# Kernel optimization log

Hardware: AMD Instinct MI355X
Metric: run time of the kernel (lower is better)

Reference implementation:

```python
import jax, jax.numpy as jnp
import numpy as np

WS_H, WS_W = 8, 8
SHIFT = 4
HEADS = 4
DIM = 128
N_DISP = 2
HEAD_DIM = DIM // HEADS
SCALE = HEAD_DIM ** -0.5
B, H, W = 4, 128, 128
M = WS_H * WS_W * N_DISP  # tokens per window = 128
NUM_WIN = (H // WS_H) * (W // WS_W)  # 256 windows per image


def _rel_pos_index():
    coords = np.stack(np.meshgrid(np.arange(WS_H), np.arange(WS_W), indexing='ij'))  # [2,wh,ww]
    cf = coords.reshape(2, -1)
    rel = (cf[:, :, None] - cf[:, None, :]).transpose(1, 2, 0).astype(np.int64)
    rel[..., 0] += WS_H - 1
    rel[..., 1] += WS_W - 1
    rel[..., 0] *= 2 * WS_W - 1
    return rel.sum(-1).astype(np.int32)  # [64,64]


def _attn_mask():
    # shifted-window mask (Swin-style) per gen_shift_window_attn_mask
    img = np.zeros((H, W), np.float32)
    h_sl = [(0, H - WS_H), (H - WS_H, H - SHIFT), (H - SHIFT, H)]
    w_sl = [(0, W - WS_W), (W - WS_W, W - SHIFT), (W - SHIFT, W)]
    cnt = 0
    for a, b in h_sl:
        for c, d in w_sl:
            img[a:b, c:d] = cnt
            cnt += 1
    mw = img.reshape(H // WS_H, WS_H, W // WS_W, WS_W).transpose(0, 2, 1, 3).reshape(-1, WS_H * WS_W)
    am = mw[:, None, :] - mw[:, :, None]  # [nw,64,64]
    am = np.where(am != 0, -np.inf, 0.0).astype(np.float32)
    am = np.repeat(np.repeat(am, N_DISP, axis=1), N_DISP, axis=2)  # [nw,128,128]
    # same-pixel (different candidate) block: -inf off-diagonal, 0 on diagonal
    idx = np.repeat(np.arange(WS_H * WS_W, dtype=np.float32), N_DISP)
    wm = np.where((idx[:, None] - idx[None, :]) == 0, -np.inf, 0.0)
    np.fill_diagonal(wm, 0.0)
    return (am + wm[None]).astype(np.float32)


def _partition(x):
    # [B,H,W,N,C] -> [B*nw, heads, wh*ww*N, head_dim]
    b, ht, wd, n, c = x.shape
    i, j = ht // WS_H, wd // WS_W
    x = x.reshape(b, i, WS_H, j, WS_W, n, HEADS, c // HEADS)
    x = x.transpose(0, 1, 3, 6, 2, 4, 5, 7)  # b,i,j,h,wh,ww,n,d
    return x.reshape(b * i * j, HEADS, WS_H * WS_W * n, c // HEADS)


def _unpartition(x, b, ht, wd, n):
    i, j = ht // WS_H, wd // WS_W
    d = x.shape[-1]
    x = x.reshape(b, i, j, HEADS, WS_H, WS_W, n, d)
    x = x.transpose(0, 1, 4, 2, 5, 6, 3, 7)  # b,i,wh,j,ww,n,h,d
    return x.reshape(b, ht, wd, n, HEADS * d)


def setup_inputs() -> dict:
    key = jax.random.key(0)
    k1, k2 = jax.random.split(key)
    qkv = jax.random.normal(k1, (B, H, W, N_DISP, 3 * DIM), dtype=jnp.float32)
    rpe_table = jax.random.normal(k2, ((2 * WS_H - 1) * (2 * WS_W - 1), 3 * DIM), dtype=jnp.float32) * 0.02
    return {
        'qkv': qkv,
        'attn_mask': jnp.asarray(_attn_mask()),
        'rpe_table': rpe_table,
        'rel_pos_index': jnp.asarray(_rel_pos_index()),
    }


def reference(qkv, attn_mask, rpe_table, rel_pos_index):
    b, ht, wd, n, _ = qkv.shape
    qkv = jnp.roll(qkv, (-SHIFT, -SHIFT), axis=(1, 2))
    q, k, v = jnp.split(qkv, 3, axis=-1)
    q, k, v = _partition(q), _partition(k), _partition(v)  # [BW,h,M,d]
    # gathered relative-position encodings -> q/k/v biases
    rpe = rpe_table[rel_pos_index.reshape(-1)].reshape(WS_H * WS_W, WS_H * WS_W, HEADS, 3 * HEAD_DIM)
    rpe = jnp.repeat(jnp.repeat(rpe, n, axis=0), n, axis=1)  # [M,M,h,3d]
    q_embed, k_embed, v_embed = jnp.split(rpe, 3, axis=-1)
    q = q * SCALE
    q_embed = q_embed * SCALE
    qk = jnp.einsum('bhic,bhjc->bhij', q, k)
    qr = jnp.einsum('bhic,ijhc->bhij', q, k_embed)
    kr = jnp.einsum('bhjc,ijhc->bhij', k, q_embed)
    attn = qk + qr + kr  # [B*nw,h,M,M]
    attn = attn.reshape(b, NUM_WIN, HEADS, M, M) + attn_mask[None, :, None, :, :]
    attn = jax.nn.softmax(attn, axis=-1).reshape(b * NUM_WIN, HEADS, M, M)
    x = jnp.einsum('bhij,bhjc->bhic', attn, v) + jnp.einsum('bhij,ijhc->bhic', attn, v_embed)
    x = _unpartition(x, b, ht, wd, n)
    x = jnp.roll(x, (SHIFT, SHIFT), axis=(1, 2))
    return x
```

## Files before the change

### kernel.cpp

```cpp
#include <hip/hip_runtime.h>

typedef unsigned int u32;
typedef unsigned short u16;
typedef float f32x4 __attribute__((ext_vector_type(4)));
typedef short s16x8 __attribute__((ext_vector_type(8)));

constexpr float SCALE = 0.17677669529663687f;

__device__ __forceinline__ u16 f2b(float f) {
  u32 x = __float_as_uint(f);
  return (u16)((x + 0x7fffu + ((x >> 16) & 1u)) >> 16);
}
__device__ __forceinline__ float b2f(u16 s) { return __uint_as_float(((u32)s) << 16); }
__device__ __forceinline__ u32 pk2(float lo, float hi) {
  return (u32)f2b(lo) | ((u32)f2b(hi) << 16);
}

union FU8 { s16x8 v; u32 u[4]; uint4 q; };

__device__ __forceinline__ void barrier_lds() {
  asm volatile("s_waitcnt lgkmcnt(0)" ::: "memory");
  __builtin_amdgcn_s_barrier();
}

__global__ __launch_bounds__(256) void prep_tabs(const float* __restrict__ rpe,
                                                 u16* __restrict__ tabs) {
  int id = blockIdx.x * 256 + threadIdx.x;
  if (id >= 94208) return;
  float val = 0.f;
  if (id < 61440) {
    int tbl = id / 30720;
    int r   = id % 30720;
    int h   = r / 7680;
    int rr  = r % 7680;
    int row = rr / 32, c = rr % 32;
    if (row < 225) {
      val = rpe[row * 384 + h * 96 + (tbl == 0 ? 32 : 0) + c];
      if (tbl == 1) val *= SCALE;
    }
  } else {
    int id2 = id - 61440;
    int h  = id2 / 8192;
    int r2 = id2 % 8192;
    int pp = r2 % 256;
    int c  = r2 / 256;
    if (pp < 225) val = rpe[pp * 384 + h * 96 + 64 + c];
  }
  tabs[id] = f2b(val);
}

__global__ __launch_bounds__(256, 3) void swin_mfma(
    const float* __restrict__ qkv,
    const u16*   __restrict__ tabs,
    float* __restrict__ out) {
  __shared__ __align__(16) u16 pool[25600];
  u16* const vt  = pool;
  u16* const qec = pool + 4352;
  u16* const p2b = pool + 12544;
  u16* const krt = pool + 20736;
  u32* const qec32 = (u32*)qec;
  u32* const p2b32 = (u32*)p2b;

  const int t = threadIdx.x;
  const int W = t >> 6;
  const int t64 = t & 63;
  const int li = t64 & 15, quad = t64 >> 4;
  u16* const scW = pool + 12544 + W * 2432;
  u16* const opv = pool;
  u16* const aaccW = (W < 3) ? (pool + 4352 + W * 2688) : (pool + 20736);

  int blk = blockIdx.x;
  blk = ((blk & 7) << 9) | (blk >> 3);
  const int h = blk & 3;
  const int w = blk >> 2;
  const int b = w >> 8;
  const int nw = w & 255;
  const int wi = nw >> 4, wj = nw & 15;
  const bool wi15 = (wi == 15), wj15 = (wj == 15);
  const int swl = (li & 7) << 3;

  auto tokoff = [&](int m) -> int {
    int y = (wi * 8 + (m >> 4) + 4) & 127;
    int x = (wj * 8 + ((m >> 1) & 7) + 4) & 127;
    return (((b * 128 + y) * 128 + x) * 2 + (m & 1)) * 384;
  };

  {
    int tok = t >> 1, chb = (t & 1) * 16;
    int vb = tokoff(tok) + 256 + h * 32 + chb;
    #pragma unroll
    for (int g = 0; g < 4; ++g) {
      float4 v4 = *(const float4*)(qkv + vb + g * 4);
      vt[(chb + g * 4 + 0) * 136 + tok] = f2b(v4.x);
      vt[(chb + g * 4 + 1) * 136 + tok] = f2b(v4.y);
      vt[(chb + g * 4 + 2) * 136 + tok] = f2b(v4.z);
      vt[(chb + g * 4 + 3) * 136 + tok] = f2b(v4.w);
    }
  }
  FU8 qf[2];
  #pragma unroll
  for (int g = 0; g < 2; ++g) {
    int base = tokoff((2 * W + g) * 16 + li) + h * 32 + quad * 8;
    float4 a = *(const float4*)(qkv + base);
    float4 c = *(const float4*)(qkv + base + 4);
    qf[g].u[0] = pk2(a.x * SCALE, a.y * SCALE);
    qf[g].u[1] = pk2(a.z * SCALE, a.w * SCALE);
    qf[g].u[2] = pk2(c.x * SCALE, c.y * SCALE);
    qf[g].u[3] = pk2(c.z * SCALE, c.w * SCALE);
  }
  FU8 kf[8];
  #pragma unroll
  for (int js = 0; js < 8; ++js) {
    int kb = tokoff(js * 16 + li) + 128 + h * 32 + quad * 8;
    float4 a = *(const float4*)(qkv + kb);
    float4 c = *(const float4*)(qkv + kb + 4);
    kf[js].u[0] = pk2(a.x, a.y); kf[js].u[1] = pk2(a.z, a.w);
    kf[js].u[2] = pk2(c.x, c.y); kf[js].u[3] = pk2(c.z, c.w);
  }

  const f32x4 zf = {0.f, 0.f, 0.f, 0.f};

  #pragma unroll
  for (int g = 0; g < 2; ++g) {
    int ss = 2 * W + g;
    int t0 = (15 * ss) >> 4;
    #pragma unroll
    for (int tt = 0; tt < 9; ++tt) {
      int pt = t0 + tt;
      FU8 bf;
      bf.q = *(const uint4*)(tabs + h * 7680 + (pt * 16 + li) * 32 + quad * 8);
      f32x4 acc = __builtin_amdgcn_mfma_f32_16x16x32_bf16(qf[g].v, bf.v, zf, 0, 0, 0);
      int rb = (quad * 4) * 152 + tt * 16 + li;
      scW[rb] = f2b(acc[0]); scW[rb + 152] = f2b(acc[1]);
      scW[rb + 304] = f2b(acc[2]); scW[rb + 456] = f2b(acc[3]);
    }
    int pbase = (ss + 7) * 15 + (li >> 1) + 7;
    int co = t0 * 16;
    int row = ss * 16 + li;
    #pragma unroll
    for (int g2 = 0; g2 < 8; ++g2) {
      int j64 = quad * 16 + 2 * g2;
      int p0 = pbase - 15 * (j64 >> 3) - (j64 & 7);
      int p1 = pbase - 15 * ((j64 + 1) >> 3) - ((j64 + 1) & 7);
      u32 lo = scW[li * 152 + (p0 - co)];
      u32 hi = scW[li * 152 + (p1 - co)];
      qec32[row * 32 + ((j64 ^ swl) >> 1)] = lo | (hi << 16);
    }
  }

  FU8 bfA, bfB, bfC;
  bfC.q = make_uint4(0, 0, 0, 0);
  {
    const int t0k = (7 * 15) >> 4;
    const u16* tq = tabs + 30720 + h * 7680;
    bfA.q = *(const uint4*)(tq + ((t0k + W) * 16 + li) * 32 + quad * 8);
    bfB.q = *(const uint4*)(tq + ((t0k + W + 4) * 16 + li) * 32 + quad * 8);
    if (W == 0) bfC.q = *(const uint4*)(tq + ((t0k + 8) * 16 + li) * 32 + quad * 8);
  }

  barrier_lds();

  f32x4 ot[2][2] = {{zf, zf}, {zf, zf}};
  float lsum[2] = {0.f, 0.f};
  const int rx_i = wj15 ? (((li >> 1) < 4) ? 1 : 2) : 0;
  u32 ppk[2][2] = {{0, 0}, {0, 0}};

  #pragma unroll
  for (int js = 0; js < 8; ++js) {
    const int cok = (((7 - js) * 15) >> 4) * 16;
    u16* const kbuf = krt + (js & 1) * 2432;
    {
      f32x4 acc = __builtin_amdgcn_mfma_f32_16x16x32_bf16(kf[js].v, bfA.v, zf, 0, 0, 0);
      int rb = (quad * 4) * 152 + W * 16 + li;
      kbuf[rb] = f2b(acc[0]); kbuf[rb + 152] = f2b(acc[1]);
      kbuf[rb + 304] = f2b(acc[2]); kbuf[rb + 456] = f2b(acc[3]);
      acc = __builtin_amdgcn_mfma_f32_16x16x32_bf16(kf[js].v, bfB.v, zf, 0, 0, 0);
      rb = (quad * 4) * 152 + (W + 4) * 16 + li;
      kbuf[rb] = f2b(acc[0]); kbuf[rb + 152] = f2b(acc[1]);
      kbuf[rb + 304] = f2b(acc[2]); kbuf[rb + 456] = f2b(acc[3]);
      if (W == (js & 3)) {
        acc = __builtin_amdgcn_mfma_f32_16x16x32_bf16(kf[js].v, bfC.v, zf, 0, 0, 0);
        rb = (quad * 4) * 152 + 128 + li;
        kbuf[rb] = f2b(acc[0]); kbuf[rb + 152] = f2b(acc[1]);
        kbuf[rb + 304] = f2b(acc[2]); kbuf[rb + 456] = f2b(acc[3]);
      }
    }
    if (js < 7) {
      const int t0n = ((7 - (js + 1)) * 15) >> 4;
      const u16* tq = tabs + 30720 + h * 7680;
      bfA.q = *(const uint4*)(tq + ((t0n + W) * 16 + li) * 32 + quad * 8);
      bfB.q = *(const uint4*)(tq + ((t0n + W + 4) * 16 + li) * 32 + quad * 8);
      if (W == ((js + 1) & 3))
        bfC.q = *(const uint4*)(tq + ((t0n + 8) * 16 + li) * 32 + quad * 8);
    }
    barrier_lds();

    __builtin_amdgcn_s_setprio(1);
    const int ry_j = wi15 ? ((js < 4) ? 1 : 2) : 0;
    u32 cpk[2][2];
    #pragma unroll
    for (int g = 0; g < 2; ++g) {
      const int it = 2 * W + g;
      f32x4 s = __builtin_amdgcn_mfma_f32_16x16x32_bf16(kf[js].v, qf[g].v, zf, 0, 0, 0);
      const int ry_i = wi15 ? ((it < 4) ? 1 : 2) : 0;
      const int i = it * 16 + li;
      const int pbq = (it + 7) * 15 + (li >> 1) + 7 - 15 * js;
      u32 qe2 = qec32[i * 32 + (((js * 8 + 2 * quad) ^ swl) >> 1)];
      float qeL = b2f((u16)qe2), qeH = b2f((u16)(qe2 >> 16));
      float e[4];
      #pragma unroll
      for (int reg = 0; reg < 4; ++reg) {
        int jl = quad * 4 + reg;
        int jw = jl >> 1;
        int rx_j = wj15 ? ((jw < 4) ? 1 : 2) : 0;
        float v = s[reg] + b2f(kbuf[jl * 152 + (pbq - jw - cok)]) +
                  ((reg < 2) ? qeL : qeH);
        bool open = (ry_i == ry_j) && (rx_i == rx_j) &&
                    !((it == js) && ((li >> 1) == jw) && (li != jl));
        e[reg] = open ? __expf(v) : 0.f;
      }
      float cs = e[0] + e[1] + e[2] + e[3];
      cs += __shfl_xor(cs, 16, 64);
      cs += __shfl_xor(cs, 32, 64);
      lsum[g] += cs;
      p2b32[i * 32 + (((js * 8 + 2 * quad) ^ swl) >> 1)] = pk2(e[0] + e[1], e[2] + e[3]);
      cpk[g][0] = pk2(e[0], e[1]);
      cpk[g][1] = pk2(e[2], e[3]);
    }

    if (js & 1) {
      const int pairbase = (js >> 1) * 32;
      FU8 vf0, vf1;
      vf0.q = *(const uint4*)&vt[li * 136 + pairbase + quad * 8];
      vf1.q = *(const uint4*)&vt[(16 + li) * 136 + pairbase + quad * 8];
      #pragma unroll
      for (int g = 0; g < 2; ++g) {
        FU8 pf;
        #pragma unroll
        for (int w2 = 0; w2 < 4; ++w2) {
          int srcLane = (2 * (quad & 1) + (w2 >> 1)) * 16 + li;
          u32 rp = (u32)__shfl((int)ppk[g][w2 & 1], srcLane, 64);
          u32 rc = (u32)__shfl((int)cpk[g][w2 & 1], srcLane, 64);
          pf.u[w2] = (quad < 2) ? rp : rc;
        }
        ot[0][g] = __builtin_amdgcn_mfma_f32_16x16x32_bf16(vf0.v, pf.v, ot[0][g], 0, 0, 0);
        ot[1][g] = __builtin_amdgcn_mfma_f32_16x16x32_bf16(vf1.v, pf.v, ot[1][g], 0, 0, 0);
      }
    } else {
      ppk[0][0] = cpk[0][0]; ppk[0][1] = cpk[0][1];
      ppk[1][0] = cpk[1][0]; ppk[1][1] = cpk[1][1];
    }
    __builtin_amdgcn_s_setprio(0);
  }

  barrier_lds();

  float iv[2] = {1.f / lsum[0], 1.f / lsum[1]};
  #pragma unroll
  for (int ct = 0; ct < 2; ++ct)
    #pragma unroll
    for (int g = 0; g < 2; ++g) {
      int i = (2 * W + g) * 16 + li;
      #pragma unroll
      for (int reg = 0; reg < 4; ++reg)
        opv[(ct * 16 + quad * 4 + reg) * 129 + i] = f2b(ot[ct][g][reg] * iv[g]);
    }

  #pragma unroll
  for (int g = 0; g < 2; ++g) {
    int ss = 2 * W + g;
    int t0 = (15 * ss) >> 4;
    int kb0 = (t0 & ~1) * 16;
    #pragma unroll
    for (int k = 0; k < 6; ++k) {
      int idx = k * 64 + t64;
      if (idx < 336) ((uint4*)aaccW)[idx] = make_uint4(0, 0, 0, 0);
    }
    int i = ss * 16 + li;
    int pbase = (ss + 7) * 15 + (li >> 1) + 7;
    #pragma unroll
    for (int g2 = 0; g2 < 8; ++g2) {
      int j64 = quad * 16 + 2 * g2;
      u32 ps = p2b32[i * 32 + ((j64 ^ swl) >> 1)];
      int p0 = pbase - 15 * (j64 >> 3) - (j64 & 7);
      int p1 = pbase - 15 * ((j64 + 1) >> 3) - ((j64 + 1) & 7);
      aaccW[li * 168 + (p0 - kb0)] = (u16)ps;
      aaccW[li * 168 + (p1 - kb0)] = (u16)(ps >> 16);
    }
    f32x4 xa0 = zf, xa1 = zf;
    #pragma unroll
    for (int kt = 0; kt < 5; ++kt) {
      FU8 af, bf0, bf1;
      af.q = *(const uint4*)&aaccW[li * 168 + kt * 32 + quad * 8];
      bf0.q = *(const uint4*)(tabs + 61440 + h * 8192 + li * 256 + kb0 + kt * 32 + quad * 8);
      bf1.q = *(const uint4*)(tabs + 61440 + h * 8192 + (16 + li) * 256 + kb0 + kt * 32 + quad * 8);
      xa0 = __builtin_amdgcn_mfma_f32_16x16x32_bf16(af.v, bf0.v, xa0, 0, 0, 0);
      xa1 = __builtin_amdgcn_mfma_f32_16x16x32_bf16(af.v, bf1.v, xa1, 0, 0, 0);
    }
    #pragma unroll
    for (int reg = 0; reg < 4; ++reg) {
      int irow = ss * 16 + quad * 4 + reg;
      float ivr = __shfl(iv[g], quad * 4 + reg, 64);
      int y = (wi * 8 + (irow >> 4) + 4) & 127;
      int x = (wj * 8 + ((irow >> 1) & 7) + 4) & 127;
      int ob = (((b * 128 + y) * 128 + x) * 2 + (irow & 1)) * 128 + h * 32;
      out[ob + li] = b2f(opv[li * 129 + irow]) + xa0[reg] * ivr;
      out[ob + 16 + li] = b2f(opv[(16 + li) * 129 + irow]) + xa1[reg] * ivr;
    }
  }
}

extern "C" void kernel_launch(void* const* d_in, const int* in_sizes, int n_in,
                              void* d_out, int out_size, void* d_ws, size_t ws_size,
                              hipStream_t stream) {
  const float* qkv = (const float*)d_in[0];
  const float* rpe = (const float*)d_in[2];
  u16* tabs = (u16*)d_ws;

  prep_tabs<<<368, 256, 0, stream>>>(rpe, tabs);
  swin_mfma<<<4096, 256, 0, stream>>>(qkv, tabs, (float*)d_out);
}
```

Measured before the change: 400.1 us.

## Keep q-embed and probability sums in registers, per-wave k-embed, shrink LDS

```diff
diff --git a/kernel.cpp b/kernel.cpp
--- a/kernel.cpp
+++ b/kernel.cpp
@@ -4,6 +4,13 @@
 typedef unsigned short u16;
 typedef float f32x4 __attribute__((ext_vector_type(4)));
 typedef short s16x8 __attribute__((ext_vector_type(8)));
+typedef u32 __attribute__((ext_vector_type(4))) u32x4;
+
+typedef u16 __attribute__((may_alias)) u16a;
+typedef u32 __attribute__((may_alias)) u32a;
+typedef u32x4 __attribute__((may_alias)) u32x4a;
+
+#define CFENCE() asm volatile("" ::: "memory")
 
 constexpr float SCALE = 0.17677669529663687f;
 
@@ -16,7 +23,7 @@
   return (u32)f2b(lo) | ((u32)f2b(hi) << 16);
 }
 
-union FU8 { s16x8 v; u32 u[4]; uint4 q; };
+union FU8 { s16x8 v; u32 u[4]; u32x4 q; };
 
 __device__ __forceinline__ void barrier_lds() {
   asm volatile("s_waitcnt lgkmcnt(0)" ::: "memory");
@@ -49,25 +56,21 @@
   tabs[id] = f2b(val);
 }
 
-__global__ __launch_bounds__(256, 3) void swin_mfma(
+__global__ __launch_bounds__(256, 4) void swin_mfma(
     const float* __restrict__ qkv,
     const u16*   __restrict__ tabs,
     float* __restrict__ out) {
-  __shared__ __align__(16) u16 pool[25600];
-  u16* const vt  = pool;
-  u16* const qec = pool + 4352;
-  u16* const p2b = pool + 12544;
-  u16* const krt = pool + 20736;
-  u32* const qec32 = (u32*)qec;
-  u32* const p2b32 = (u32*)p2b;
+  __shared__ __align__(16) u16 pool[15104];
+  u16a* const vt  = (u16a*)pool;
+  u32a* const vt32 = (u32a*)pool;
 
   const int t = threadIdx.x;
   const int W = t >> 6;
   const int t64 = t & 63;
   const int li = t64 & 15, quad = t64 >> 4;
-  u16* const scW = pool + 12544 + W * 2432;
-  u16* const opv = pool;
-  u16* const aaccW = (W < 3) ? (pool + 4352 + W * 2688) : (pool + 20736);
+  u16a* const wreg = (u16a*)(pool + 4352 + W * 2688);
+  u32a* const wreg32 = (u32a*)wreg;
+  u16a* const opv = (u16a*)pool;
 
   int blk = blockIdx.x;
   blk = ((blk & 7) << 9) | (blk >> 3);
@@ -77,7 +80,6 @@
   const int nw = w & 255;
   const int wi = nw >> 4, wj = nw & 15;
   const bool wi15 = (wi == 15), wj15 = (wj == 15);
-  const int swl = (li & 7) << 3;
 
   auto tokoff = [&](int m) -> int {
     int y = (wi * 8 + (m >> 4) + 4) & 127;
@@ -86,27 +88,34 @@
   };
 
   {
-    int tok = t >> 1, chb = (t & 1) * 16;
-    int vb = tokoff(tok) + 256 + h * 32 + chb;
-    #pragma unroll
-    for (int g = 0; g < 4; ++g) {
-      float4 v4 = *(const float4*)(qkv + vb + g * 4);
-      vt[(chb + g * 4 + 0) * 136 + tok] = f2b(v4.x);
-      vt[(chb + g * 4 + 1) * 136 + tok] = f2b(v4.y);
-      vt[(chb + g * 4 + 2) * 136 + tok] = f2b(v4.z);
-      vt[(chb + g * 4 + 3) * 136 + tok] = f2b(v4.w);
-    }
-  }
+    int p = t64;
+    int ch0 = W * 8;
+    int vb = tokoff(2 * p) + 256 + h * 32 + ch0;
+    float4 a0 = *(const float4*)(qkv + vb);
+    float4 a1 = *(const float4*)(qkv + vb + 4);
+    float4 c0 = *(const float4*)(qkv + vb + 384);
+    float4 c1 = *(const float4*)(qkv + vb + 388);
+    vt32[(ch0 + 0) * 68 + p] = pk2(a0.x, c0.x);
+    vt32[(ch0 + 1) * 68 + p] = pk2(a0.y, c0.y);
+    vt32[(ch0 + 2) * 68 + p] = pk2(a0.z, c0.z);
+    vt32[(ch0 + 3) * 68 + p] = pk2(a0.w, c0.w);
+    vt32[(ch0 + 4) * 68 + p] = pk2(a1.x, c1.x);
+    vt32[(ch0 + 5) * 68 + p] = pk2(a1.y, c1.y);
+    vt32[(ch0 + 6) * 68 + p] = pk2(a1.z, c1.z);
+    vt32[(ch0 + 7) * 68 + p] = pk2(a1.w, c1.w);
+  }
+
+  const float QS = SCALE;
   FU8 qf[2];
   #pragma unroll
   for (int g = 0; g < 2; ++g) {
     int base = tokoff((2 * W + g) * 16 + li) + h * 32 + quad * 8;
     float4 a = *(const float4*)(qkv + base);
     float4 c = *(const float4*)(qkv + base + 4);
-    qf[g].u[0] = pk2(a.x * SCALE, a.y * SCALE);
-    qf[g].u[1] = pk2(a.z * SCALE, a.w * SCALE);
-    qf[g].u[2] = pk2(c.x * SCALE, c.y * SCALE);
-    qf[g].u[3] = pk2(c.z * SCALE, c.w * SCALE);
+    qf[g].u[0] = pk2(a.x * QS, a.y * QS);
+    qf[g].u[1] = pk2(a.z * QS, a.w * QS);
+    qf[g].u[2] = pk2(c.x * QS, c.y * QS);
+    qf[g].u[3] = pk2(c.z * QS, c.w * QS);
   }
   FU8 kf[8];
   #pragma unroll
@@ -120,82 +129,58 @@
 
   const f32x4 zf = {0.f, 0.f, 0.f, 0.f};
 
+  u32 qe[2][8];
   #pragma unroll
   for (int g = 0; g < 2; ++g) {
     int ss = 2 * W + g;
     int t0 = (15 * ss) >> 4;
+    CFENCE();
     #pragma unroll
     for (int tt = 0; tt < 9; ++tt) {
-      int pt = t0 + tt;
       FU8 bf;
-      bf.q = *(const uint4*)(tabs + h * 7680 + (pt * 16 + li) * 32 + quad * 8);
+      bf.q = *(const u32x4*)(tabs + h * 7680 + ((t0 + tt) * 16 + li) * 32 + quad * 8);
       f32x4 acc = __builtin_amdgcn_mfma_f32_16x16x32_bf16(qf[g].v, bf.v, zf, 0, 0, 0);
-      int rb = (quad * 4) * 152 + tt * 16 + li;
-      scW[rb] = f2b(acc[0]); scW[rb + 152] = f2b(acc[1]);
-      scW[rb + 304] = f2b(acc[2]); scW[rb + 456] = f2b(acc[3]);
-    }
+      u32 idx = (u32)((tt * 16 + li) * 9 + 2 * quad);
+      wreg32[idx] = pk2(acc[0], acc[1]);
+      wreg32[idx + 1] = pk2(acc[2], acc[3]);
+    }
+    CFENCE();
     int pbase = (ss + 7) * 15 + (li >> 1) + 7;
     int co = t0 * 16;
-    int row = ss * 16 + li;
-    #pragma unroll
-    for (int g2 = 0; g2 < 8; ++g2) {
-      int j64 = quad * 16 + 2 * g2;
-      int p0 = pbase - 15 * (j64 >> 3) - (j64 & 7);
-      int p1 = pbase - 15 * ((j64 + 1) >> 3) - ((j64 + 1) & 7);
-      u32 lo = scW[li * 152 + (p0 - co)];
-      u32 hi = scW[li * 152 + (p1 - co)];
-      qec32[row * 32 + ((j64 ^ swl) >> 1)] = lo | (hi << 16);
-    }
-  }
-
-  FU8 bfA, bfB, bfC;
-  bfC.q = make_uint4(0, 0, 0, 0);
-  {
-    const int t0k = (7 * 15) >> 4;
-    const u16* tq = tabs + 30720 + h * 7680;
-    bfA.q = *(const uint4*)(tq + ((t0k + W) * 16 + li) * 32 + quad * 8);
-    bfB.q = *(const uint4*)(tq + ((t0k + W + 4) * 16 + li) * 32 + quad * 8);
-    if (W == 0) bfC.q = *(const uint4*)(tq + ((t0k + 8) * 16 + li) * 32 + quad * 8);
+    #pragma unroll
+    for (int js = 0; js < 8; ++js) {
+      int p0 = pbase - 15 * js - 2 * quad;
+      u32 lo = wreg[(p0 - co) * 18 + li];
+      u32 hi = wreg[(p0 - 1 - co) * 18 + li];
+      qe[g][js] = lo | (hi << 16);
+    }
   }
 
   barrier_lds();
 
   f32x4 ot[2][2] = {{zf, zf}, {zf, zf}};
   float lsum[2] = {0.f, 0.f};
+  u32 pp[2][8];
+  u32 ppk[2][2] = {{0, 0}, {0, 0}};
   const int rx_i = wj15 ? (((li >> 1) < 4) ? 1 : 2) : 0;
-  u32 ppk[2][2] = {{0, 0}, {0, 0}};
 
   #pragma unroll
   for (int js = 0; js < 8; ++js) {
-    const int cok = (((7 - js) * 15) >> 4) * 16;
-    u16* const kbuf = krt + (js & 1) * 2432;
-    {
-      f32x4 acc = __builtin_amdgcn_mfma_f32_16x16x32_bf16(kf[js].v, bfA.v, zf, 0, 0, 0);
-      int rb = (quad * 4) * 152 + W * 16 + li;
-      kbuf[rb] = f2b(acc[0]); kbuf[rb + 152] = f2b(acc[1]);
-      kbuf[rb + 304] = f2b(acc[2]); kbuf[rb + 456] = f2b(acc[3]);
-      acc = __builtin_amdgcn_mfma_f32_16x16x32_bf16(kf[js].v, bfB.v, zf, 0, 0, 0);
-      rb = (quad * 4) * 152 + (W + 4) * 16 + li;
-      kbuf[rb] = f2b(acc[0]); kbuf[rb + 152] = f2b(acc[1]);
-      kbuf[rb + 304] = f2b(acc[2]); kbuf[rb + 456] = f2b(acc[3]);
-      if (W == (js & 3)) {
-        acc = __builtin_amdgcn_mfma_f32_16x16x32_bf16(kf[js].v, bfC.v, zf, 0, 0, 0);
-        rb = (quad * 4) * 152 + 128 + li;
-        kbuf[rb] = f2b(acc[0]); kbuf[rb + 152] = f2b(acc[1]);
-        kbuf[rb + 304] = f2b(acc[2]); kbuf[rb + 456] = f2b(acc[3]);
-      }
-    }
-    if (js < 7) {
-      const int t0n = ((7 - (js + 1)) * 15) >> 4;
-      const u16* tq = tabs + 30720 + h * 7680;
-      bfA.q = *(const uint4*)(tq + ((t0n + W) * 16 + li) * 32 + quad * 8);
-      bfB.q = *(const uint4*)(tq + ((t0n + W + 4) * 16 + li) * 32 + quad * 8);
-      if (W == ((js + 1) & 3))
-        bfC.q = *(const uint4*)(tq + ((t0n + 8) * 16 + li) * 32 + quad * 8);
-    }
-    barrier_lds();
-
-    __builtin_amdgcn_s_setprio(1);
+    const int pw0 = 15 * (2 * W + 7 - js);
+    const int pt0 = pw0 >> 4;
+    const int cok = pt0 * 16;
+    CFENCE();
+    #pragma unroll
+    for (int k = 0; k < 3; ++k) {
+      FU8 bf;
+      bf.q = *(const u32x4*)(tabs + 30720 + h * 7680 + ((pt0 + k) * 16 + li) * 32 + quad * 8);
+      f32x4 acc = __builtin_amdgcn_mfma_f32_16x16x32_bf16(kf[js].v, bf.v, zf, 0, 0, 0);
+      u32 idx = (u32)((k * 16 + li) * 9 + 2 * quad);
+      wreg32[idx] = pk2(acc[0], acc[1]);
+      wreg32[idx + 1] = pk2(acc[2], acc[3]);
+    }
+    CFENCE();
+
     const int ry_j = wi15 ? ((js < 4) ? 1 : 2) : 0;
     u32 cpk[2][2];
     #pragma unroll
@@ -203,27 +188,27 @@
       const int it = 2 * W + g;
       f32x4 s = __builtin_amdgcn_mfma_f32_16x16x32_bf16(kf[js].v, qf[g].v, zf, 0, 0, 0);
       const int ry_i = wi15 ? ((it < 4) ? 1 : 2) : 0;
-      const int i = it * 16 + li;
       const int pbq = (it + 7) * 15 + (li >> 1) + 7 - 15 * js;
-      u32 qe2 = qec32[i * 32 + (((js * 8 + 2 * quad) ^ swl) >> 1)];
-      float qeL = b2f((u16)qe2), qeH = b2f((u16)(qe2 >> 16));
+      const float qeL = b2f((u16)qe[g][js]);
+      const float qeH = b2f((u16)(qe[g][js] >> 16));
       float e[4];
       #pragma unroll
       for (int reg = 0; reg < 4; ++reg) {
         int jl = quad * 4 + reg;
         int jw = jl >> 1;
         int rx_j = wj15 ? ((jw < 4) ? 1 : 2) : 0;
-        float v = s[reg] + b2f(kbuf[jl * 152 + (pbq - jw - cok)]) +
+        float v = s[reg] + b2f(wreg[(pbq - jw - cok) * 18 + jl]) +
                   ((reg < 2) ? qeL : qeH);
         bool open = (ry_i == ry_j) && (rx_i == rx_j) &&
                     !((it == js) && ((li >> 1) == jw) && (li != jl));
         e[reg] = open ? __expf(v) : 0.f;
       }
-      float cs = e[0] + e[1] + e[2] + e[3];
+      float a01 = e[0] + e[1], a23 = e[2] + e[3];
+      float cs = a01 + a23;
       cs += __shfl_xor(cs, 16, 64);
       cs += __shfl_xor(cs, 32, 64);
       lsum[g] += cs;
-      p2b32[i * 32 + (((js * 8 + 2 * quad) ^ swl) >> 1)] = pk2(e[0] + e[1], e[2] + e[3]);
+      pp[g][js] = pk2(a01, a23);
       cpk[g][0] = pk2(e[0], e[1]);
       cpk[g][1] = pk2(e[2], e[3]);
     }
@@ -231,8 +216,8 @@
     if (js & 1) {
       const int pairbase = (js >> 1) * 32;
       FU8 vf0, vf1;
-      vf0.q = *(const uint4*)&vt[li * 136 + pairbase + quad * 8];
-      vf1.q = *(const uint4*)&vt[(16 + li) * 136 + pairbase + quad * 8];
+      vf0.q = *(const u32x4a*)&vt[li * 136 + pairbase + quad * 8];
+      vf1.q = *(const u32x4a*)&vt[(16 + li) * 136 + pairbase + quad * 8];
       #pragma unroll
       for (int g = 0; g < 2; ++g) {
         FU8 pf;
@@ -250,7 +235,6 @@
       ppk[0][0] = cpk[0][0]; ppk[0][1] = cpk[0][1];
       ppk[1][0] = cpk[1][0]; ppk[1][1] = cpk[1][1];
     }
-    __builtin_amdgcn_s_setprio(0);
   }
 
   barrier_lds();
@@ -271,29 +255,28 @@
     int ss = 2 * W + g;
     int t0 = (15 * ss) >> 4;
     int kb0 = (t0 & ~1) * 16;
+    CFENCE();
     #pragma unroll
     for (int k = 0; k < 6; ++k) {
       int idx = k * 64 + t64;
-      if (idx < 336) ((uint4*)aaccW)[idx] = make_uint4(0, 0, 0, 0);
-    }
-    int i = ss * 16 + li;
+      if (idx < 336) ((u32x4a*)wreg)[idx] = (u32x4){0, 0, 0, 0};
+    }
+    CFENCE();
     int pbase = (ss + 7) * 15 + (li >> 1) + 7;
     #pragma unroll
-    for (int g2 = 0; g2 < 8; ++g2) {
-      int j64 = quad * 16 + 2 * g2;
-      u32 ps = p2b32[i * 32 + ((j64 ^ swl) >> 1)];
-      int p0 = pbase - 15 * (j64 >> 3) - (j64 & 7);
-      int p1 = pbase - 15 * ((j64 + 1) >> 3) - ((j64 + 1) & 7);
-      aaccW[li * 168 + (p0 - kb0)] = (u16)ps;
-      aaccW[li * 168 + (p1 - kb0)] = (u16)(ps >> 16);
-    }
+    for (int js = 0; js < 8; ++js) {
+      int p0 = pbase - 15 * js - 2 * quad;
+      wreg[li * 168 + (p0 - kb0)] = (u16)pp[g][js];
+      wreg[li * 168 + (p0 - 1 - kb0)] = (u16)(pp[g][js] >> 16);
+    }
+    CFENCE();
     f32x4 xa0 = zf, xa1 = zf;
     #pragma unroll
     for (int kt = 0; kt < 5; ++kt) {
       FU8 af, bf0, bf1;
-      af.q = *(const uint4*)&aaccW[li * 168 + kt * 32 + quad * 8];
-      bf0.q = *(const uint4*)(tabs + 61440 + h * 8192 + li * 256 + kb0 + kt * 32 + quad * 8);
-      bf1.q = *(const uint4*)(tabs + 61440 + h * 8192 + (16 + li) * 256 + kb0 + kt * 32 + quad * 8);
+      af.q = *(const u32x4a*)&wreg[li * 168 + kt * 32 + quad * 8];
+      bf0.q = *(const u32x4*)(tabs + 61440 + h * 8192 + li * 256 + kb0 + kt * 32 + quad * 8);
+      bf1.q = *(const u32x4*)(tabs + 61440 + h * 8192 + (16 + li) * 256 + kb0 + kt * 32 + quad * 8);
       xa0 = __builtin_amdgcn_mfma_f32_16x16x32_bf16(af.v, bf0.v, xa0, 0, 0, 0);
       xa1 = __builtin_amdgcn_mfma_f32_16x16x32_bf16(af.v, bf1.v, xa1, 0, 0, 0);
     }
```

New measurement: 458.4 us. +14.6%, slower.
